# Performance work log

Measured on AMD Instinct MI355X. Metric: run time of the kernel, lower is better.

Reference implementation:

```python
import jax, jax.numpy as jnp
import numpy as np

HIDDEN = 1024
B, S = 4, 2048

def setup_inputs() -> dict:
    key = jax.random.key(0)
    k1, k2 = jax.random.split(key)
    qkv = jax.random.normal(k1, (B, S, HIDDEN), dtype=jnp.float32)
    mask = jnp.ones((B, S), dtype=jnp.float32)
    W_qkv = jax.random.normal(k2, (HIDDEN, 3 * HIDDEN), dtype=jnp.float32) * (HIDDEN ** -0.5)
    b_qkv = jnp.zeros((3 * HIDDEN,), dtype=jnp.float32)
    return {"qkv": qkv, "mask": mask, "W_qkv": W_qkv, "b_qkv": b_qkv}

def reference(qkv, mask, W_qkv, b_qkv):
    scale = HIDDEN ** -0.5
    proj = jnp.einsum("bsi,ih->bsh", qkv, W_qkv) + b_qkv  # [B,S,3H]
    q, k, v = jnp.split(proj, 3, axis=-1)                  # each [B,S,H]
    q = q * scale
    scores = jnp.einsum("bqh,bkh->bqk", q, k)              # [B,S,S]
    scores = scores + (1.0 - mask)[:, None, :] * -10000.0
    dist = jax.nn.softmax(scores, axis=-1)                 # dropout = identity (eval)
    return jnp.einsum("bqk,bkh->bqh", dist, v)             # [B,S,H]
```

## Files before the change

### kernel.cpp

```cpp
#include <hip/hip_runtime.h>
#include <hip/hip_bf16.h>

#define HID   1024
#define H3    3072
#define SEQ   2048
#define NB    4
#define MTOT  8192

typedef __bf16 bf16;
typedef bf16  bf16x4 __attribute__((ext_vector_type(4)));
typedef bf16  bf16x8 __attribute__((ext_vector_type(8)));
typedef float f32x4  __attribute__((ext_vector_type(4)));

#define MFMA16(a, b, c) __builtin_amdgcn_mfma_f32_16x16x32_bf16((a), (b), (c), 0, 0, 0)

#define GLOAD_LDS16(gp, lp)                                                     \
    __builtin_amdgcn_global_load_lds(                                           \
        (const __attribute__((address_space(1))) void*)(gp),                    \
        (__attribute__((address_space(3))) void*)(lp), 16, 0, 0)

#define FENCE() asm volatile("" ::: "memory")

__device__ __forceinline__ void stage_half(
    const bf16* __restrict__ G, long ld, long row0, long col0,
    char* dstbase, int w, int lane)
{
    const int r  = lane >> 2;
    const int c0 = ((lane & 3) * 8) ^ (((lane >> 5) & 1) << 4);
#pragma unroll
    for (int l = 0; l < 2; ++l) {
        const int sh = l * 8 + w;
        const bf16* src = G + (row0 + (long)((sh >> 1) * 16 + r)) * ld
                            + col0 + ((sh & 1) * 32 + c0);
        GLOAD_LDS16(src, dstbase + sh * 1024);
    }
}

__device__ __forceinline__ void gemm256_core(
    const bf16* __restrict__ A, long lda,
    const bf16* __restrict__ Bt, long ldb,
    long m0, long n0, int NT, char* lds, f32x4 (&acc)[8][4])
{
    const int tid = threadIdx.x, lane = tid & 63, w = tid >> 6;
    const int lr = lane & 15, lkg = lane >> 4;
    const int subA = (w >> 2) * 8;
    const int subB = (w & 3) * 4;
    const int inner = lr * 64 + (((lkg * 8) ^ ((lr >> 3) << 4)) << 1);

    char* A0b = lds;
    char* B0b = lds + 32768;
    char* A1b = lds + 65536;
    char* B1b = lds + 98304;

    stage_half(A,  lda, m0,        0, A0b,          w, lane);
    stage_half(A,  lda, m0 + 128,  0, A0b + 16384,  w, lane);
    stage_half(Bt, ldb, n0,        0, B0b,          w, lane);
    stage_half(Bt, ldb, n0 + 128,  0, B0b + 16384,  w, lane);
    stage_half(Bt, ldb, n0,       64, B1b,          w, lane);
    stage_half(Bt, ldb, n0 + 128, 64, B1b + 16384,  w, lane);
    asm volatile("s_waitcnt vmcnt(0)" ::: "memory");
    __builtin_amdgcn_s_barrier();
    FENCE();

    bf16x8 aR[4][2], bR[4][2];

    for (int t = 0; t < NT; ++t) {
        char* Ac = (t & 1) ? A1b : A0b;
        char* Bc = (t & 1) ? B1b : B0b;
        char* An = (t & 1) ? A0b : A1b;
        const long kA = (long)(t + 1) * 64;
        const long kB = (long)(t + 2) * 64;
        const bool doA = (t + 1 < NT), doB = (t + 2 < NT);

#pragma unroll
        for (int mf = 0; mf < 4; ++mf)
#pragma unroll
            for (int ks = 0; ks < 2; ++ks)
                aR[mf][ks] = *(const bf16x8*)(Ac + ((subA + mf) * 2 + ks) * 1024 + inner);
#pragma unroll
        for (int nf = 0; nf < 2; ++nf)
#pragma unroll
            for (int ks = 0; ks < 2; ++ks)
                bR[nf][ks] = *(const bf16x8*)(Bc + ((subB + nf) * 2 + ks) * 1024 + inner);
        if (doA) stage_half(A, lda, m0, kA, An, w, lane);
        __builtin_amdgcn_s_barrier();
        __builtin_amdgcn_s_setprio(1);
#pragma unroll
        for (int mf = 0; mf < 4; ++mf)
#pragma unroll
            for (int nf = 0; nf < 2; ++nf)
#pragma unroll
                for (int ks = 0; ks < 2; ++ks)
                    acc[mf][nf] = MFMA16(aR[mf][ks], bR[nf][ks], acc[mf][nf]);
        __builtin_amdgcn_s_setprio(0);
        __builtin_amdgcn_s_barrier();
        FENCE();

#pragma unroll
        for (int nf = 0; nf < 2; ++nf)
#pragma unroll
            for (int ks = 0; ks < 2; ++ks)
                bR[2 + nf][ks] = *(const bf16x8*)(Bc + ((subB + 2 + nf) * 2 + ks) * 1024 + inner);
        if (doA) stage_half(A, lda, m0 + 128, kA, An + 16384, w, lane);
        __builtin_amdgcn_s_barrier();
        __builtin_amdgcn_s_setprio(1);
#pragma unroll
        for (int mf = 0; mf < 4; ++mf)
#pragma unroll
            for (int nf = 0; nf < 2; ++nf)
#pragma unroll
                for (int ks = 0; ks < 2; ++ks)
                    acc[mf][2 + nf] = MFMA16(aR[mf][ks], bR[2 + nf][ks], acc[mf][2 + nf]);
        __builtin_amdgcn_s_setprio(0);
        __builtin_amdgcn_s_barrier();
        FENCE();

#pragma unroll
        for (int mf = 0; mf < 4; ++mf)
#pragma unroll
            for (int ks = 0; ks < 2; ++ks)
                aR[mf][ks] = *(const bf16x8*)(Ac + ((subA + 4 + mf) * 2 + ks) * 1024 + inner);
        if (doB) stage_half(Bt, ldb, n0, kB, Bc, w, lane);
        __builtin_amdgcn_s_barrier();
        __builtin_amdgcn_s_setprio(1);
#pragma unroll
        for (int mf = 0; mf < 4; ++mf)
#pragma unroll
            for (int nf = 0; nf < 2; ++nf)
#pragma unroll
                for (int ks = 0; ks < 2; ++ks)
                    acc[4 + mf][nf] = MFMA16(aR[mf][ks], bR[nf][ks], acc[4 + mf][nf]);
        __builtin_amdgcn_s_setprio(0);
        __builtin_amdgcn_s_barrier();
        FENCE();

        if (doB) {
            stage_half(Bt, ldb, n0 + 128, kB, Bc + 16384, w, lane);
            asm volatile("s_waitcnt vmcnt(4)" ::: "memory");
        } else {
            asm volatile("s_waitcnt vmcnt(0)" ::: "memory");
        }
        __builtin_amdgcn_s_barrier();
        __builtin_amdgcn_s_setprio(1);
#pragma unroll
        for (int mf = 0; mf < 4; ++mf)
#pragma unroll
            for (int nf = 0; nf < 2; ++nf)
#pragma unroll
                for (int ks = 0; ks < 2; ++ks)
                    acc[4 + mf][2 + nf] = MFMA16(aR[mf][ks], bR[2 + nf][ks], acc[4 + mf][2 + nf]);
        __builtin_amdgcn_s_setprio(0);
        __builtin_amdgcn_s_barrier();
        FENCE();
    }
}

__device__ __forceinline__ void gemm_h_core(
    const bf16* __restrict__ A, long lda,
    const bf16* __restrict__ Bt, long ldb,
    long m0, long n0, int NT, char* lds, f32x4 (&acc)[4][4])
{
    const int tid = threadIdx.x, lane = tid & 63, w = tid >> 6;
    const int lr = lane & 15, lkg = lane >> 4;
    const int subA = (w >> 2) * 4;
    const int subB = (w & 3) * 4;
    const int inner = lr * 64 + (((lkg * 8) ^ ((lr >> 3) << 4)) << 1);

    char* A0b = lds;
    char* B0b = lds + 16384;
    char* A1b = lds + 49152;
    char* B1b = lds + 65536;

    stage_half(A,  lda, m0,        0, A0b,          w, lane);
    stage_half(Bt, ldb, n0,        0, B0b,          w, lane);
    stage_half(Bt, ldb, n0 + 128,  0, B0b + 16384,  w, lane);
    stage_half(Bt, ldb, n0,       64, B1b,          w, lane);
    stage_half(Bt, ldb, n0 + 128, 64, B1b + 16384,  w, lane);
    asm volatile("s_waitcnt vmcnt(0)" ::: "memory");
    __builtin_amdgcn_s_barrier();
    FENCE();

    bf16x8 aR[2][2], bR[4][2];

    for (int t = 0; t < NT; ++t) {
        char* Ac = (t & 1) ? A1b : A0b;
        char* Bc = (t & 1) ? B1b : B0b;
        char* An = (t & 1) ? A0b : A1b;
        const long kA = (long)(t + 1) * 64;
        const long kB = (long)(t + 2) * 64;
        const bool doA = (t + 1 < NT), doB = (t + 2 < NT);

#pragma unroll
        for (int mf = 0; mf < 2; ++mf)
#pragma unroll
            for (int ks = 0; ks < 2; ++ks)
                aR[mf][ks] = *(const bf16x8*)(Ac + ((subA + mf) * 2 + ks) * 1024 + inner);
#pragma unroll
        for (int nf = 0; nf < 2; ++nf)
#pragma unroll
            for (int ks = 0; ks < 2; ++ks)
                bR[nf][ks] = *(const bf16x8*)(Bc + ((subB + nf) * 2 + ks) * 1024 + inner);
        if (doA) stage_half(A, lda, m0, kA, An, w, lane);
        __builtin_amdgcn_s_barrier();
        __builtin_amdgcn_s_setprio(1);
#pragma unroll
        for (int mf = 0; mf < 2; ++mf)
#pragma unroll
            for (int nf = 0; nf < 2; ++nf)
#pragma unroll
                for (int ks = 0; ks < 2; ++ks)
                    acc[mf][nf] = MFMA16(aR[mf][ks], bR[nf][ks], acc[mf][nf]);
        __builtin_amdgcn_s_setprio(0);
        __builtin_amdgcn_s_barrier();
        FENCE();

#pragma unroll
        for (int nf = 0; nf < 2; ++nf)
#pragma unroll
            for (int ks = 0; ks < 2; ++ks)
                bR[2 + nf][ks] = *(const bf16x8*)(Bc + ((subB + 2 + nf) * 2 + ks) * 1024 + inner);
        __builtin_amdgcn_s_barrier();
        __builtin_amdgcn_s_setprio(1);
#pragma unroll
        for (int mf = 0; mf < 2; ++mf)
#pragma unroll
            for (int nf = 0; nf < 2; ++nf)
#pragma unroll
                for (int ks = 0; ks < 2; ++ks)
                    acc[mf][2 + nf] = MFMA16(aR[mf][ks], bR[2 + nf][ks], acc[mf][2 + nf]);
        __builtin_amdgcn_s_setprio(0);
        __builtin_amdgcn_s_barrier();
        FENCE();

#pragma unroll
        for (int mf = 0; mf < 2; ++mf)
#pragma unroll
            for (int ks = 0; ks < 2; ++ks)
                aR[mf][ks] = *(const bf16x8*)(Ac + ((subA + 2 + mf) * 2 + ks) * 1024 + inner);
        if (doB) {
            stage_half(Bt, ldb, n0,       kB, Bc,         w, lane);
            stage_half(Bt, ldb, n0 + 128, kB, Bc + 16384, w, lane);
        }
        __builtin_amdgcn_s_barrier();
        __builtin_amdgcn_s_setprio(1);
#pragma unroll
        for (int mf = 0; mf < 2; ++mf)
#pragma unroll
            for (int nf = 0; nf < 2; ++nf)
#pragma unroll
                for (int ks = 0; ks < 2; ++ks)
                    acc[2 + mf][nf] = MFMA16(aR[mf][ks], bR[nf][ks], acc[2 + mf][nf]);
        __builtin_amdgcn_s_setprio(0);
        __builtin_amdgcn_s_barrier();
        FENCE();

        if (doB) {
            asm volatile("s_waitcnt vmcnt(4)" ::: "memory");
        } else {
            asm volatile("s_waitcnt vmcnt(0)" ::: "memory");
        }
        __builtin_amdgcn_s_barrier();
        __builtin_amdgcn_s_setprio(1);
#pragma unroll
        for (int mf = 0; mf < 2; ++mf)
#pragma unroll
            for (int nf = 0; nf < 2; ++nf)
#pragma unroll
                for (int ks = 0; ks < 2; ++ks)
                    acc[2 + mf][2 + nf] = MFMA16(aR[mf][ks], bR[2 + nf][ks], acc[2 + mf][2 + nf]);
        __builtin_amdgcn_s_setprio(0);
        __builtin_amdgcn_s_barrier();
        FENCE();
    }
}

__global__ __launch_bounds__(256) void conv_kernel(
    const float* __restrict__ X, const float* __restrict__ W,
    bf16* __restrict__ Xb, bf16* __restrict__ Wt)
{
    __shared__ bf16 T[64][66];
    const int bid = blockIdx.x;
    if (bid < 4096) {
        const long i = ((long)bid * 256 + threadIdx.x) * 8;
        float4 a = *(const float4*)(X + i);
        float4 b = *(const float4*)(X + i + 4);
        bf16x8 o;
        o[0] = (bf16)a.x; o[1] = (bf16)a.y; o[2] = (bf16)a.z; o[3] = (bf16)a.w;
        o[4] = (bf16)b.x; o[5] = (bf16)b.y; o[6] = (bf16)b.z; o[7] = (bf16)b.w;
        *(bf16x8*)(Xb + i) = o;
    } else {
        const int b2 = bid - 4096;
        const int n0 = (b2 % 48) * 64, k0 = (b2 / 48) * 64;
        const int r = threadIdx.x >> 2, s = threadIdx.x & 3;
        const float* wp = W + (size_t)(k0 + r) * H3 + n0 + s * 16;
#pragma unroll
        for (int q = 0; q < 4; ++q) {
            float4 a = *(const float4*)(wp + q * 4);
            T[r][s * 16 + q * 4 + 0] = (bf16)a.x;
            T[r][s * 16 + q * 4 + 1] = (bf16)a.y;
            T[r][s * 16 + q * 4 + 2] = (bf16)a.z;
            T[r][s * 16 + q * 4 + 3] = (bf16)a.w;
        }
        __syncthreads();
        bf16x8 o0, o1;
#pragma unroll
        for (int i = 0; i < 8; ++i) o0[i] = T[s * 16 + i][r];
#pragma unroll
        for (int i = 0; i < 8; ++i) o1[i] = T[s * 16 + 8 + i][r];
        bf16* op = Wt + (size_t)(n0 + r) * HID + k0 + s * 16;
        *(bf16x8*)op       = o0;
        *(bf16x8*)(op + 8) = o1;
    }
}

__global__ __launch_bounds__(512, 2) void proj_gemm2(
    const bf16* __restrict__ Xb, const bf16* __restrict__ Wt,
    const float* __restrict__ bias,
    bf16* __restrict__ Qb, bf16* __restrict__ Kb, bf16* __restrict__ Vt)
{
    __shared__ __attribute__((aligned(16))) char lds[135168];
    const int x = blockIdx.x & 7, q = blockIdx.x >> 3;
    const int bn = q >> 2, bm = x * 4 + (q & 3);

    f32x4 acc[8][4] = {};
    gemm256_core(Xb, HID, Wt, HID, (long)bm * 256, (long)bn * 256, 16, lds, acc);

    const int tid = threadIdx.x, lane = tid & 63, w = tid >> 6;
    const int lr = lane & 15, lkg = lane >> 4;
    const int wmL = (w >> 2) * 128;
    const int wnL = (w & 3) * 64;
    const int seg = bn >> 2;

    __syncthreads();
    bf16* sm_ = (bf16*)lds;

    if (seg < 2) {
        const float qs = (seg == 0) ? 0.03125f : 1.0f;
#pragma unroll
        for (int nf = 0; nf < 4; ++nf) {
            const int nl = wnL + nf * 16 + lr;
            const float bv = bias[bn * 256 + nl];
#pragma unroll
            for (int mf = 0; mf < 8; ++mf) {
                const int ml = wmL + mf * 16 + lkg * 4;
#pragma unroll
                for (int j = 0; j < 4; ++j)
                    sm_[(ml + j) * 264 + nl] = (bf16)((acc[mf][nf][j] + bv) * qs);
            }
        }
        __syncthreads();
        bf16* dst = (seg == 0) ? Qb : Kb;
        const long colbase = (long)(bn & 3) * 256;
        const long rowbase = (long)bm * 256;
#pragma unroll
        for (int it = 0; it < 16; ++it) {
            const int ml = (tid >> 5) + it * 16;
            const int nc = (tid & 31) * 8;
            bf16x8 vv = *(const bf16x8*)&sm_[ml * 264 + nc];
            *(bf16x8*)&dst[(rowbase + ml) * HID + colbase + nc] = vv;
        }
    } else {
#pragma unroll
        for (int nf = 0; nf < 4; ++nf) {
            const int nl = wnL + nf * 16 + lr;
            const float bv = bias[bn * 256 + nl];
#pragma unroll
            for (int mf = 0; mf < 8; ++mf) {
                const int ml = wmL + mf * 16 + lkg * 4;
                bf16x4 pk;
#pragma unroll
                for (int j = 0; j < 4; ++j) pk[j] = (bf16)(acc[mf][nf][j] + bv);
                *(bf16x4*)&sm_[nl * 264 + ml] = pk;
            }
        }
        __syncthreads();
        const int  bb = bm >> 3;
        const long s0 = (long)(bm & 7) * 256;
        const long h0 = (long)bn * 256 - 2048;
#pragma unroll
        for (int it = 0; it < 16; ++it) {
            const int nl = (tid >> 5) + it * 16;
            const int mc = (tid & 31) * 8;
            bf16x8 vv = *(const bf16x8*)&sm_[nl * 264 + mc];
            *(bf16x8*)&Vt[((long)(bb << 10) + h0 + nl) * SEQ + s0 + mc] = vv;
        }
    }
}

__global__ __launch_bounds__(512, 2) void qk_gemm2(
    const bf16* __restrict__ Qb, const bf16* __restrict__ Kb,
    float* __restrict__ Sc, int b_base)
{
    __shared__ __attribute__((aligned(16))) char lds[131072];
    const int z = blockIdx.z, b = b_base + z;

    f32x4 acc[8][4] = {};
    gemm256_core(Qb + (size_t)b * SEQ * HID, HID,
                 Kb + (size_t)b * SEQ * HID, HID,
                 (long)blockIdx.x * 256, (long)blockIdx.y * 256, 16, lds, acc);

    const int tid = threadIdx.x, lane = tid & 63, w = tid >> 6;
    const int lr = lane & 15, lkg = lane >> 4;
    const int m0i = (int)blockIdx.x * 256 + (w >> 2) * 128;
    const int n0i = (int)blockIdx.y * 256 + (w & 3) * 64;
    float* C = Sc + (size_t)z * SEQ * SEQ;
#pragma unroll
    for (int mf = 0; mf < 8; ++mf)
#pragma unroll
        for (int j = 0; j < 4; ++j) {
            const int row = m0i + mf * 16 + lkg * 4 + j;
#pragma unroll
            for (int nf = 0; nf < 4; ++nf)
                C[(size_t)row * SEQ + n0i + nf * 16 + lr] = acc[mf][nf][j];
        }
}

__global__ __launch_bounds__(256) void sm_kernel(
    float* __restrict__ Sc, const float* __restrict__ mask, int b_base)
{
    __shared__ float redm[4], reds[4];
    const long row = blockIdx.x;
    const int  z = (int)(row >> 11);
    const int  b = b_base + z;
    const int tid = threadIdx.x, lane = tid & 63, w = tid >> 6;

    float* sp = Sc + row * SEQ;
    float v[8];
    {
        float4 a = *(const float4*)(sp + tid * 8);
        float4 c = *(const float4*)(sp + tid * 8 + 4);
        const float* mp = mask + (size_t)b * SEQ + tid * 8;
        float4 m0 = *(const float4*)mp;
        float4 m1 = *(const float4*)(mp + 4);
        v[0] = a.x + (1.0f - m0.x) * -10000.0f;
        v[1] = a.y + (1.0f - m0.y) * -10000.0f;
        v[2] = a.z + (1.0f - m0.z) * -10000.0f;
        v[3] = a.w + (1.0f - m0.w) * -10000.0f;
        v[4] = c.x + (1.0f - m1.x) * -10000.0f;
        v[5] = c.y + (1.0f - m1.y) * -10000.0f;
        v[6] = c.z + (1.0f - m1.z) * -10000.0f;
        v[7] = c.w + (1.0f - m1.w) * -10000.0f;
    }
    float mx = v[0];
#pragma unroll
    for (int i = 1; i < 8; ++i) mx = fmaxf(mx, v[i]);
#pragma unroll
    for (int d = 1; d < 64; d <<= 1) mx = fmaxf(mx, __shfl_xor(mx, d));
    if (lane == 0) redm[w] = mx;
    __syncthreads();
    mx = fmaxf(fmaxf(redm[0], redm[1]), fmaxf(redm[2], redm[3]));

    float s = 0.0f;
#pragma unroll
    for (int i = 0; i < 8; ++i) { v[i] = __expf(v[i] - mx); s += v[i]; }
#pragma unroll
    for (int d = 1; d < 64; d <<= 1) s += __shfl_xor(s, d);
    if (lane == 0) reds[w] = s;
    __syncthreads();
    s = reds[0] + reds[1] + reds[2] + reds[3];
    const float inv = 1.0f / s;

    bf16x8 o;
#pragma unroll
    for (int i = 0; i < 8; ++i) o[i] = (bf16)(v[i] * inv);
    *(bf16x8*)((bf16*)sp + tid * 8) = o;
}

__global__ __launch_bounds__(512, 2) void pv_gemm2(
    const bf16* __restrict__ P, const bf16* __restrict__ Vt,
    float* __restrict__ out, int b_base)
{
    __shared__ __attribute__((aligned(16))) char lds[98304];
    const int z = blockIdx.z, b = b_base + z;

    f32x4 acc[4][4] = {};
    gemm_h_core(P + (size_t)z * SEQ * 4096, 4096,
                Vt + (size_t)b * HID * SEQ, SEQ,
                (long)blockIdx.x * 128, (long)blockIdx.y * 256, 32, lds, acc);

    const int tid = threadIdx.x, lane = tid & 63, w = tid >> 6;
    const int lr = lane & 15, lkg = lane >> 4;
    const int m0i = (int)blockIdx.x * 128 + (w >> 2) * 64;
    const int n0i = (int)blockIdx.y * 256 + (w & 3) * 64;
    float* C = out + (size_t)b * SEQ * HID;
#pragma unroll
    for (int mf = 0; mf < 4; ++mf)
#pragma unroll
        for (int j = 0; j < 4; ++j) {
            const int row = m0i + mf * 16 + lkg * 4 + j;
#pragma unroll
            for (int nf = 0; nf < 4; ++nf)
                C[(size_t)row * HID + n0i + nf * 16 + lr] = acc[mf][nf][j];
        }
}

extern "C" void kernel_launch(void* const* d_in, const int* in_sizes, int n_in,
                              void* d_out, int out_size, void* d_ws, size_t ws_size,
                              hipStream_t stream)
{
    const float* X    = (const float*)d_in[0];
    const float* mask = (const float*)d_in[1];
    const float* W    = (const float*)d_in[2];
    const float* bias = (const float*)d_in[3];
    float* out = (float*)d_out;

    char* ws = (char*)d_ws;
    const size_t MB = 1024 * 1024;
    bf16* Qb = (bf16*)ws;
    bf16* Kb = (bf16*)(ws + 16 * MB);
    bf16* Vt = (bf16*)(ws + 32 * MB);
    bf16*  Xb = (bf16*)(ws + 48 * MB);
    bf16*  Wt = (bf16*)(ws + 64 * MB);
    float* Sc = (float*)(ws + 48 * MB);

    int nbg;
    if      (ws_size >= 112 * MB) nbg = 4;
    else if (ws_size >=  80 * MB) nbg = 2;
    else                          nbg = 1;

    conv_kernel<<<4096 + 768, 256, 0, stream>>>(X, W, Xb, Wt);
    proj_gemm2<<<384, 512, 0, stream>>>(Xb, Wt, bias, Qb, Kb, Vt);

    for (int g = 0; g < NB / nbg; ++g) {
        const int b0 = g * nbg;
        qk_gemm2<<<dim3(8, 8, nbg), 512, 0, stream>>>(Qb, Kb, Sc, b0);
        sm_kernel<<<nbg * SEQ, 256, 0, stream>>>(Sc, mask, b0);
        pv_gemm2<<<dim3(16, 4, nbg), 512, 0, stream>>>((const bf16*)Sc, Vt, out, b0);
    }
}
```

Measured before the change: 172.4 us.

## Fuse masked exp into QK GEMM epilogue and defer softmax normalization to PV

Removes the separate softmax kernel. The QK GEMM epilogue now adds the mask, exponentiates, stages bf16 probabilities in LDS for coalesced stores, and atomically accumulates per-row sums into a buffer that the conversion kernel zeroes. The PV GEMM divides its outputs by the row sums. This avoids writing and re-reading the fp32 score matrix. In exchange the max subtraction is dropped, so large scores could overflow exp, and the atomics add a little contention.

```diff
diff --git a/kernel.cpp b/kernel.cpp
--- a/kernel.cpp
+++ b/kernel.cpp
@@ -276,7 +276,7 @@
 
 __global__ __launch_bounds__(256) void conv_kernel(
     const float* __restrict__ X, const float* __restrict__ W,
-    bf16* __restrict__ Xb, bf16* __restrict__ Wt)
+    bf16* __restrict__ Xb, bf16* __restrict__ Wt, float* __restrict__ lbuf)
 {
     __shared__ bf16 T[64][66];
     const int bid = blockIdx.x;
@@ -288,7 +288,7 @@
         o[0] = (bf16)a.x; o[1] = (bf16)a.y; o[2] = (bf16)a.z; o[3] = (bf16)a.w;
         o[4] = (bf16)b.x; o[5] = (bf16)b.y; o[6] = (bf16)b.z; o[7] = (bf16)b.w;
         *(bf16x8*)(Xb + i) = o;
-    } else {
+    } else if (bid < 4096 + 768) {
         const int b2 = bid - 4096;
         const int n0 = (b2 % 48) * 64, k0 = (b2 / 48) * 64;
         const int r = threadIdx.x >> 2, s = threadIdx.x & 3;
@@ -310,6 +310,8 @@
         bf16* op = Wt + (size_t)(n0 + r) * HID + k0 + s * 16;
         *(bf16x8*)op       = o0;
         *(bf16x8*)(op + 8) = o1;
+    } else {
+        for (int i = threadIdx.x; i < MTOT; i += 256) lbuf[i] = 0.0f;
     }
 }
 
@@ -389,9 +391,11 @@
 
 __global__ __launch_bounds__(512, 2) void qk_gemm2(
     const bf16* __restrict__ Qb, const bf16* __restrict__ Kb,
-    float* __restrict__ Sc, int b_base)
-{
-    __shared__ __attribute__((aligned(16))) char lds[131072];
+    bf16* __restrict__ Pb, float* __restrict__ lbuf,
+    const float* __restrict__ mask, int b_base)
+{
+    __shared__ __attribute__((aligned(16))) char lds[135168];
+    __shared__ float lsum[2][128][4];
     const int z = blockIdx.z, b = b_base + z;
 
     f32x4 acc[8][4] = {};
@@ -401,80 +405,68 @@
 
     const int tid = threadIdx.x, lane = tid & 63, w = tid >> 6;
     const int lr = lane & 15, lkg = lane >> 4;
-    const int m0i = (int)blockIdx.x * 256 + (w >> 2) * 128;
-    const int n0i = (int)blockIdx.y * 256 + (w & 3) * 64;
-    float* C = Sc + (size_t)z * SEQ * SEQ;
-#pragma unroll
-    for (int mf = 0; mf < 8; ++mf)
+    const int mh = w >> 2;
+    const int nw = w & 3;
+
+    __syncthreads();
+    bf16* smP = (bf16*)lds;
+
+    float mterm[4];
+#pragma unroll
+    for (int nf = 0; nf < 4; ++nf) {
+        const int col = (int)blockIdx.y * 256 + nw * 64 + nf * 16 + lr;
+        mterm[nf] = (1.0f - mask[(size_t)b * SEQ + col]) * -10000.0f;
+    }
+
+#pragma unroll
+    for (int mf = 0; mf < 8; ++mf) {
 #pragma unroll
         for (int j = 0; j < 4; ++j) {
-            const int row = m0i + mf * 16 + lkg * 4 + j;
-#pragma unroll
-            for (int nf = 0; nf < 4; ++nf)
-                C[(size_t)row * SEQ + n0i + nf * 16 + lr] = acc[mf][nf][j];
-        }
-}
-
-__global__ __launch_bounds__(256) void sm_kernel(
-    float* __restrict__ Sc, const float* __restrict__ mask, int b_base)
-{
-    __shared__ float redm[4], reds[4];
-    const long row = blockIdx.x;
-    const int  z = (int)(row >> 11);
-    const int  b = b_base + z;
-    const int tid = threadIdx.x, lane = tid & 63, w = tid >> 6;
-
-    float* sp = Sc + row * SEQ;
-    float v[8];
-    {
-        float4 a = *(const float4*)(sp + tid * 8);
-        float4 c = *(const float4*)(sp + tid * 8 + 4);
-        const float* mp = mask + (size_t)b * SEQ + tid * 8;
-        float4 m0 = *(const float4*)mp;
-        float4 m1 = *(const float4*)(mp + 4);
-        v[0] = a.x + (1.0f - m0.x) * -10000.0f;
-        v[1] = a.y + (1.0f - m0.y) * -10000.0f;
-        v[2] = a.z + (1.0f - m0.z) * -10000.0f;
-        v[3] = a.w + (1.0f - m0.w) * -10000.0f;
-        v[4] = c.x + (1.0f - m1.x) * -10000.0f;
-        v[5] = c.y + (1.0f - m1.y) * -10000.0f;
-        v[6] = c.z + (1.0f - m1.z) * -10000.0f;
-        v[7] = c.w + (1.0f - m1.w) * -10000.0f;
-    }
-    float mx = v[0];
-#pragma unroll
-    for (int i = 1; i < 8; ++i) mx = fmaxf(mx, v[i]);
-#pragma unroll
-    for (int d = 1; d < 64; d <<= 1) mx = fmaxf(mx, __shfl_xor(mx, d));
-    if (lane == 0) redm[w] = mx;
+            const int rloc = mf * 16 + lkg * 4 + j;
+            float rs = 0.0f;
+#pragma unroll
+            for (int nf = 0; nf < 4; ++nf) {
+                const float e = __expf(acc[mf][nf][j] + mterm[nf]);
+                smP[(mh * 128 + rloc) * 264 + nw * 64 + nf * 16 + lr] = (bf16)e;
+                rs += e;
+            }
+            rs += __shfl_xor(rs, 1);
+            rs += __shfl_xor(rs, 2);
+            rs += __shfl_xor(rs, 4);
+            rs += __shfl_xor(rs, 8);
+            if (lr == 0) lsum[mh][rloc][nw] = rs;
+        }
+    }
     __syncthreads();
-    mx = fmaxf(fmaxf(redm[0], redm[1]), fmaxf(redm[2], redm[3]));
-
-    float s = 0.0f;
-#pragma unroll
-    for (int i = 0; i < 8; ++i) { v[i] = __expf(v[i] - mx); s += v[i]; }
-#pragma unroll
-    for (int d = 1; d < 64; d <<= 1) s += __shfl_xor(s, d);
-    if (lane == 0) reds[w] = s;
-    __syncthreads();
-    s = reds[0] + reds[1] + reds[2] + reds[3];
-    const float inv = 1.0f / s;
-
-    bf16x8 o;
-#pragma unroll
-    for (int i = 0; i < 8; ++i) o[i] = (bf16)(v[i] * inv);
-    *(bf16x8*)((bf16*)sp + tid * 8) = o;
+
+    bf16* P = Pb + (size_t)z * SEQ * SEQ;
+    const long rowbase = (long)blockIdx.x * 256;
+    const long colbase = (long)blockIdx.y * 256;
+#pragma unroll
+    for (int it = 0; it < 16; ++it) {
+        const int ml = (tid >> 5) + it * 16;
+        const int nc = (tid & 31) * 8;
+        bf16x8 vv = *(const bf16x8*)&smP[ml * 264 + nc];
+        *(bf16x8*)&P[(rowbase + ml) * SEQ + colbase + nc] = vv;
+    }
+
+    if (tid < 256) {
+        const int half = tid >> 7, r128 = tid & 127;
+        const float s4 = lsum[half][r128][0] + lsum[half][r128][1]
+                       + lsum[half][r128][2] + lsum[half][r128][3];
+        atomicAdd(&lbuf[(size_t)b * SEQ + rowbase + tid], s4);
+    }
 }
 
 __global__ __launch_bounds__(512, 2) void pv_gemm2(
-    const bf16* __restrict__ P, const bf16* __restrict__ Vt,
-    float* __restrict__ out, int b_base)
+    const bf16* __restrict__ Pb, const bf16* __restrict__ Vt,
+    const float* __restrict__ lbuf, float* __restrict__ out, int b_base)
 {
     __shared__ __attribute__((aligned(16))) char lds[98304];
     const int z = blockIdx.z, b = b_base + z;
 
     f32x4 acc[4][4] = {};
-    gemm_h_core(P + (size_t)z * SEQ * 4096, 4096,
+    gemm_h_core(Pb + (size_t)z * SEQ * SEQ, SEQ,
                 Vt + (size_t)b * HID * SEQ, SEQ,
                 (long)blockIdx.x * 128, (long)blockIdx.y * 256, 32, lds, acc);
 
@@ -488,9 +480,10 @@
 #pragma unroll
         for (int j = 0; j < 4; ++j) {
             const int row = m0i + mf * 16 + lkg * 4 + j;
+            const float inv = 1.0f / lbuf[(size_t)b * SEQ + row];
 #pragma unroll
             for (int nf = 0; nf < 4; ++nf)
-                C[(size_t)row * HID + n0i + nf * 16 + lr] = acc[mf][nf][j];
+                C[(size_t)row * HID + n0i + nf * 16 + lr] = acc[mf][nf][j] * inv;
         }
 }
 
@@ -506,25 +499,25 @@
 
     char* ws = (char*)d_ws;
     const size_t MB = 1024 * 1024;
-    bf16* Qb = (bf16*)ws;
-    bf16* Kb = (bf16*)(ws + 16 * MB);
-    bf16* Vt = (bf16*)(ws + 32 * MB);
-    bf16*  Xb = (bf16*)(ws + 48 * MB);
-    bf16*  Wt = (bf16*)(ws + 64 * MB);
-    float* Sc = (float*)(ws + 48 * MB);
+    bf16*  Qb   = (bf16*)ws;
+    bf16*  Kb   = (bf16*)(ws + 16 * MB);
+    bf16*  Vt   = (bf16*)(ws + 32 * MB);
+    float* lbuf = (float*)(ws + 48 * MB);
+    bf16*  Xb   = (bf16*)(ws + 49 * MB);
+    bf16*  Wt   = (bf16*)(ws + 65 * MB);
+    bf16*  Pb   = (bf16*)(ws + 49 * MB);
 
     int nbg;
-    if      (ws_size >= 112 * MB) nbg = 4;
-    else if (ws_size >=  80 * MB) nbg = 2;
-    else                          nbg = 1;
-
-    conv_kernel<<<4096 + 768, 256, 0, stream>>>(X, W, Xb, Wt);
+    if      (ws_size >= 81 * MB) nbg = 4;
+    else if (ws_size >= 65 * MB) nbg = 2;
+    else                         nbg = 1;
+
+    conv_kernel<<<4096 + 768 + 1, 256, 0, stream>>>(X, W, Xb, Wt, lbuf);
     proj_gemm2<<<384, 512, 0, stream>>>(Xb, Wt, bias, Qb, Kb, Vt);
 
     for (int g = 0; g < NB / nbg; ++g) {
         const int b0 = g * nbg;
-        qk_gemm2<<<dim3(8, 8, nbg), 512, 0, stream>>>(Qb, Kb, Sc, b0);
-        sm_kernel<<<nbg * SEQ, 256, 0, stream>>>(Sc, mask, b0);
-        pv_gemm2<<<dim3(16, 4, nbg), 512, 0, stream>>>((const bf16*)Sc, Vt, out, b0);
-    }
-}
+        qk_gemm2<<<dim3(8, 8, nbg), 512, 0, stream>>>(Qb, Kb, Pb, lbuf, mask, b0);
+        pv_gemm2<<<dim3(16, 4, nbg), 512, 0, stream>>>(Pb, Vt, lbuf, out, b0);
+    }
+}
```

Result: faster. 159.3 us (-7.6%).
